# Optimization experiments

Measured on AMD Instinct MI355X. Metric: run time of the kernel, lower is better.

## Reference

```python
import jax, jax.numpy as jnp
import numpy as np

LMAX = 3
D_IRREP = (LMAX + 1) ** 2  # 16
EPS = 1e-5


def _conv1d(x, w, pad):
    # x: [N, C_in, L], w: [C_out, C_in, K] -> [N, C_out, L]
    return jax.lax.conv_general_dilated(
        x, w, window_strides=(1,), padding=[(pad, pad)],
        dimension_numbers=("NCH", "OIH", "NCH"))


def setup_inputs() -> dict:
    key = jax.random.key(0)
    ks = jax.random.split(key, 8)
    B, Cin, Cout, N, K, RES = 128, 256, 256, 64, 5, 8
    return {
        "x": jax.random.normal(ks[0], (B, Cin * D_IRREP, N), jnp.float32),
        "weight": jax.random.normal(ks[1], (LMAX + 1, Cout, Cin, K), jnp.float32) / np.sqrt(Cin * K).astype(np.float32),
        "bias": jax.random.normal(ks[2], (1, 1, Cout), jnp.float32) * 0.02,
        "affine_weight": jnp.ones((LMAX + 1, Cout), jnp.float32),
        "gating_w": jax.random.normal(ks[3], (Cout, Cout), jnp.float32) / np.sqrt(Cout).astype(np.float32),
        "gating_b": jnp.zeros((Cout,), jnp.float32),
        "to_grid": jax.random.normal(ks[4], (RES, RES, D_IRREP), jnp.float32) * 0.3,
        "from_grid": jax.random.normal(ks[5], (RES, RES, D_IRREP), jnp.float32) * 0.3,
    }


def reference(x, weight, bias, affine_weight, gating_w, gating_b, to_grid, from_grid):
    B, CI, N = x.shape
    Cin = CI // D_IRREP
    Cout = weight.shape[1]
    pad = weight.shape[-1] // 2
    x = x.reshape(B, Cin, D_IRREP, N)

    # per-degree Conv1d over the time axis, irrep order folded into batch
    h_parts = []
    for l in range(LMAX + 1):
        lo, li = l * l, 2 * l + 1
        x_l = x[:, :, lo:lo + li, :]                                  # [B, Cin, li, N]
        x_l = x_l.transpose(0, 2, 1, 3).reshape(B * li, Cin, N)       # (b i) c n
        h_l = _conv1d(x_l, weight[l], pad)                            # [B*li, Cout, N]
        h_l = h_l.reshape(B, li, Cout, N).transpose(0, 3, 1, 2).reshape(B * N, li, Cout)  # (b n) i c
        if l == 0:
            h_l = h_l + bias
        h_parts.append(h_l)
    h = jnp.concatenate(h_parts, axis=1)                              # [B*N, 16, Cout]

    # rms_norm_sh: center l=0 over channels, degree-balanced RMS, per-degree affine
    degrees = np.repeat(np.arange(LMAX + 1), 2 * np.arange(LMAX + 1) + 1)  # [16]
    bal = jnp.asarray((1.0 / (2.0 * degrees + 1.0)) / (LMAX + 1), h.dtype)  # [16]
    mean0 = jnp.mean(h[:, :1, :], axis=2, keepdims=True)
    h = jnp.concatenate([h[:, :1, :] - mean0, h[:, 1:, :]], axis=1)
    var = jnp.einsum("zic,i->zc", h * h, bal)                         # [Z, C]
    inv = jax.lax.rsqrt(jnp.mean(var, axis=-1)[:, None, None] + EPS)  # [Z,1,1]
    h = h * inv * affine_weight[degrees][None]                        # [Z,16,C]

    # SeparableS2Activation: SiLU-gated scalars + S2 grid activation for l>0
    gate = jax.nn.silu(h[:, :1, :] @ gating_w.T + gating_b)           # [Z,1,C]
    grid = jax.nn.silu(jnp.einsum("bai,zic->zbac", to_grid, h))       # [Z,8,8,C]
    s2 = jnp.einsum("bai,zbac->zic", from_grid, grid)                 # [Z,16,C]
    h = jnp.concatenate([gate, s2[:, 1:, :]], axis=1)

    # (b n) i c -> b (c i) n
    out = h.reshape(B, N, D_IRREP, Cout).transpose(0, 3, 2, 1).reshape(B, Cout * D_IRREP, N)
    return out
```

## Files before the change

### kernel.cpp

```cpp
#include <hip/hip_runtime.h>
#include <hip/hip_bf16.h>

#define BB    128
#define CIN   256
#define COUT  256
#define NN    64
#define KW    5
#define DIRR  16
#define ZTOT  (BB*NN)
#define SX    264

typedef __attribute__((ext_vector_type(4)))  float f32x4;
typedef __attribute__((ext_vector_type(16))) float f32x16;
typedef __attribute__((ext_vector_type(8)))  short s16x8;

__device__ inline ushort f2bf(float f) {
    __hip_bfloat16 h = __float2bfloat16(f);
    return *(const ushort*)&h;
}
__device__ inline float bf2f(ushort u) {
    union { unsigned int ui; float f; } cv; cv.ui = ((unsigned int)u) << 16;
    return cv.f;
}
__device__ inline float wave_sum(float v) {
    #pragma unroll
    for (int o = 32; o > 0; o >>= 1) v += __shfl_down(v, o, 64);
    return v;
}
__device__ inline float silu(float x) { return x / (1.f + __expf(-x)); }

__global__ __launch_bounds__(256) void pack_all_k(const float* __restrict__ w,
                                                  const float* __restrict__ gw,
                                                  const float* __restrict__ tg,
                                                  const float* __restrict__ fg,
                                                  ushort* __restrict__ wb,
                                                  ushort* __restrict__ gwb,
                                                  ushort* __restrict__ tgb,
                                                  ushort* __restrict__ fgTb)
{
    int idx = blockIdx.x * 256 + threadIdx.x;
    if (idx < 1310720) {
        int cl16 = idx & 15;
        int c    = (idx >> 4) & 255;
        int ch   = (idx >> 12) & 15;
        int lk   = idx >> 16;
        int k    = lk % 5;
        int l    = lk / 5;
        int cin  = ch * 16 + cl16;
        wb[idx] = f2bf(w[(((size_t)(l * COUT + c) * CIN) + cin) * KW + k]);
        return;
    }
    int j2 = idx - 1310720;
    if (j2 < 65536) {
        gwb[j2] = f2bf(gw[j2]);
    } else if (j2 < 66560) {
        int j = j2 - 65536;
        tgb[j] = f2bf(tg[j]);
    } else if (j2 < 67584) {
        int j = j2 - 66560;
        int p = j >> 4, i = j & 15;
        fgTb[i * 64 + p] = f2bf(fg[j]);
    }
}

__global__ __launch_bounds__(256, 4) void conv_mfma_k(const float* __restrict__ x,
                                                      const ushort* __restrict__ wb,
                                                      const float* __restrict__ bias,
                                                      ushort* __restrict__ hbuf)
{
    __shared__ __align__(16) ushort xs[68 * SX];

    const int tid  = threadIdx.x;
    const int lane = tid & 63;
    const int wid  = tid >> 6;
    const int blk  = blockIdx.x;
    const int b = blk >> 4, i = blk & 15;
    const int l = (i == 0) ? 0 : (i < 4) ? 1 : (i < 9) ? 2 : 3;

    {
        const float4* xb = (const float4*)(x + (((size_t)b * CIN) * DIRR + i) * NN);
        #pragma unroll
        for (int p = 0; p < 16; ++p) {
            int cin = (tid & 63) | ((p & 3) << 6);
            int nq  = ((tid >> 6) << 2) | (p >> 2);
            float4 v = xb[(size_t)cin * (DIRR * NN / 4) + nq];
            ushort* dst = xs + (size_t)(2 + nq * 4) * SX + cin;
            dst[0]      = f2bf(v.x);
            dst[SX]     = f2bf(v.y);
            dst[2 * SX] = f2bf(v.z);
            dst[3 * SX] = f2bf(v.w);
        }
        xs[ 0 * SX + tid] = 0; xs[ 1 * SX + tid] = 0;
        xs[66 * SX + tid] = 0; xs[67 * SX + tid] = 0;
    }
    __syncthreads();

    f32x16 acc[2][2];
    #pragma unroll
    for (int m = 0; m < 2; ++m)
        #pragma unroll
        for (int j = 0; j < 2; ++j)
            #pragma unroll
            for (int r = 0; r < 16; ++r) acc[m][j][r] = 0.f;

    const int l31 = lane & 31;
    const int kh  = lane >> 5;

    const ushort* wl = wb + (size_t)l * (80 * 4096);
    int boffB[2];
    #pragma unroll
    for (int j = 0; j < 2; ++j)
        boffB[j] = (wid * 64 + j * 32 + l31) * 16 + kh * 8;

    const ushort* arow = xs + (size_t)l31 * SX + kh * 8;

#define LOADB(dst, t) do {                                              \
        const ushort* bt_ = wl + ((size_t)(t) << 12);                   \
        dst##0 = *(const s16x8*)(bt_ + boffB[0]);                       \
        dst##1 = *(const s16x8*)(bt_ + boffB[1]);                       \
    } while (0)

#define MSTEP(bv, t) do {                                               \
        const ushort* ab_ = arow + (size_t)((t) >> 4) * SX + ((t) & 15) * 16; \
        s16x8 av0_ = *(const s16x8*)(ab_);                              \
        s16x8 av1_ = *(const s16x8*)(ab_ + (size_t)32 * SX);            \
        acc[0][0] = __builtin_amdgcn_mfma_f32_32x32x16_bf16(av0_, bv##0, acc[0][0], 0, 0, 0); \
        acc[0][1] = __builtin_amdgcn_mfma_f32_32x32x16_bf16(av0_, bv##1, acc[0][1], 0, 0, 0); \
        acc[1][0] = __builtin_amdgcn_mfma_f32_32x32x16_bf16(av1_, bv##0, acc[1][0], 0, 0, 0); \
        acc[1][1] = __builtin_amdgcn_mfma_f32_32x32x16_bf16(av1_, bv##1, acc[1][1], 0, 0, 0); \
    } while (0)

    s16x8 s0_0, s0_1, s1_0, s1_1, s2_0, s2_1, s3_0, s3_1;
    LOADB(s0_, 0);
    LOADB(s1_, 1);
    LOADB(s2_, 2);
    LOADB(s3_, 3);

    #pragma unroll 1
    for (int t = 0; t < 80; t += 4) {
        MSTEP(s0_, t);
        if (t + 4 < 80) LOADB(s0_, t + 4);
        MSTEP(s1_, t + 1);
        if (t + 5 < 80) LOADB(s1_, t + 5);
        MSTEP(s2_, t + 2);
        if (t + 6 < 80) LOADB(s2_, t + 6);
        MSTEP(s3_, t + 3);
        if (t + 7 < 80) LOADB(s3_, t + 7);
    }
#undef LOADB
#undef MSTEP

    #pragma unroll
    for (int j = 0; j < 2; ++j) {
        int c = wid * 64 + j * 32 + l31;
        float bvv = (i == 0) ? bias[c] : 0.f;
        #pragma unroll
        for (int m = 0; m < 2; ++m)
            #pragma unroll
            for (int r = 0; r < 16; ++r) {
                int n = m * 32 + (r & 3) + 8 * (r >> 2) + 4 * kh;
                size_t z = (size_t)b * NN + n;
                hbuf[(z * DIRR + i) * COUT + c] = f2bf(acc[m][j][r] + bvv);
            }
    }
}

__global__ __launch_bounds__(256) void norm_k(const ushort* __restrict__ hbuf,
                                              const float* __restrict__ afw,
                                              ushort* __restrict__ hn2,
                                              ushort* __restrict__ hn0)
{
    __shared__ float red[16];
    const int z0 = blockIdx.x * 4;
    const int c = threadIdx.x;
    const int lane = c & 63, w = c >> 6;

    float hv[4][16];
    #pragma unroll
    for (int zz = 0; zz < 4; ++zz)
        #pragma unroll
        for (int i = 0; i < 16; ++i)
            hv[zz][i] = bf2f(hbuf[((size_t)(z0 + zz) * DIRR + i) * COUT + c]);

    float s[4];
    #pragma unroll
    for (int zz = 0; zz < 4; ++zz) s[zz] = wave_sum(hv[zz][0]);
    if (lane == 0) {
        #pragma unroll
        for (int zz = 0; zz < 4; ++zz) red[zz * 4 + w] = s[zz];
    }
    __syncthreads();
    #pragma unroll
    for (int zz = 0; zz < 4; ++zz) {
        float m = (red[zz * 4] + red[zz * 4 + 1] + red[zz * 4 + 2] + red[zz * 4 + 3]) * (1.f / 256.f);
        hv[zz][0] -= m;
    }

    const float bal[4] = {0.25f, 1.f / 12.f, 1.f / 20.f, 1.f / 28.f};
    float var[4];
    #pragma unroll
    for (int zz = 0; zz < 4; ++zz) {
        float v = bal[0] * hv[zz][0] * hv[zz][0];
        #pragma unroll
        for (int i = 1; i < 16; ++i) {
            int li = (i < 4) ? 1 : (i < 9) ? 2 : 3;
            v += bal[li] * hv[zz][i] * hv[zz][i];
        }
        var[zz] = wave_sum(v);
    }
    __syncthreads();
    if (lane == 0) {
        #pragma unroll
        for (int zz = 0; zz < 4; ++zz) red[zz * 4 + w] = var[zz];
    }
    __syncthreads();
    float inv[4];
    #pragma unroll
    for (int zz = 0; zz < 4; ++zz)
        inv[zz] = rsqrtf((red[zz * 4] + red[zz * 4 + 1] + red[zz * 4 + 2] + red[zz * 4 + 3]) * (1.f / 256.f) + 1e-5f);

    float a0 = afw[c], a1 = afw[COUT + c], a2 = afw[2 * COUT + c], a3 = afw[3 * COUT + c];
    #pragma unroll
    for (int zz = 0; zz < 4; ++zz) {
        s16x8 o0, o1;
        #pragma unroll
        for (int i = 0; i < 16; ++i) {
            float al = (i == 0) ? a0 : (i < 4) ? a1 : (i < 9) ? a2 : a3;
            ushort ub = f2bf(hv[zz][i] * inv[zz] * al);
            if (i < 8) o0[i] = (short)ub; else o1[i - 8] = (short)ub;
        }
        ushort* dst = hn2 + ((size_t)c * ZTOT + z0 + zz) * DIRR;
        *(s16x8*)dst = o0;
        *(s16x8*)(dst + 8) = o1;
        hn0[(size_t)(z0 + zz) * COUT + c] = (ushort)(unsigned short)o0[0];
    }
}

__global__ __launch_bounds__(256) void gate_k(const ushort* __restrict__ hn0,
                                              const ushort* __restrict__ gwb,
                                              const float* __restrict__ gb,
                                              float* __restrict__ out)
{
    const int b = blockIdx.x;
    const int tid = threadIdx.x;
    const int lane = tid & 63, w = tid >> 6;
    const int lr = lane & 15, kb = lane >> 4;

    f32x4 acc[4][4];
    #pragma unroll
    for (int m = 0; m < 4; ++m)
        #pragma unroll
        for (int n = 0; n < 4; ++n) acc[m][n] = (f32x4){0.f, 0.f, 0.f, 0.f};

    #pragma unroll 1
    for (int ks = 0; ks < 8; ++ks) {
        s16x8 av[4], bv[4];
        #pragma unroll
        for (int m = 0; m < 4; ++m)
            av[m] = *(const s16x8*)(hn0 + ((size_t)(b * 64 + m * 16 + lr) * 256 + ks * 32 + kb * 8));
        #pragma unroll
        for (int n = 0; n < 4; ++n)
            bv[n] = *(const s16x8*)(gwb + ((size_t)(w * 64 + n * 16 + lr) * 256 + ks * 32 + kb * 8));
        #pragma unroll
        for (int m = 0; m < 4; ++m)
            #pragma unroll
            for (int n = 0; n < 4; ++n)
                acc[m][n] = __builtin_amdgcn_mfma_f32_16x16x32_bf16(av[m], bv[n], acc[m][n], 0, 0, 0);
    }

    #pragma unroll
    for (int n = 0; n < 4; ++n) {
        int c = w * 64 + n * 16 + lr;
        float gbc = gb[c];
        #pragma unroll
        for (int m = 0; m < 4; ++m)
            #pragma unroll
            for (int r = 0; r < 4; ++r) {
                int nrow = m * 16 + kb * 4 + r;
                out[((size_t)b * COUT + c) * (DIRR * NN) + nrow] = silu(acc[m][n][r] + gbc);
            }
    }
}

__global__ __launch_bounds__(256) void grid_k(const ushort* __restrict__ hn2,
                                              const ushort* __restrict__ tgb,
                                              const ushort* __restrict__ fgTb,
                                              float* __restrict__ out)
{
    __shared__ __align__(16) char lds[36864 + 2048 + 2304];
    ushort* P_s  = (ushort*)lds;
    float*  S_s  = (float*)lds;
    ushort* tg_s = (ushort*)(lds + 36864);
    ushort* fgT_s= (ushort*)(lds + 36864 + 2048);

    const int bid = blockIdx.x;
    const int c  = bid & 255;
    const int zt = bid >> 8;
    const int z0 = zt * 256;
    const int tid = threadIdx.x;
    const int lane = tid & 63, w = tid >> 6;
    const int lr = lane & 15, kb = lane >> 4;

    #pragma unroll
    for (int q = 0; q < 4; ++q) {
        int idx = q * 256 + tid;
        tg_s[idx] = tgb[idx];
        int i = idx >> 6, p = idx & 63;
        fgT_s[i * 72 + p] = fgTb[idx];
    }
    __syncthreads();

    f32x4 acc[4][4];
    #pragma unroll
    for (int m = 0; m < 4; ++m)
        #pragma unroll
        for (int n = 0; n < 4; ++n) acc[m][n] = (f32x4){0.f, 0.f, 0.f, 0.f};

    s16x8 bv[4];
    #pragma unroll
    for (int n = 0; n < 4; ++n)
        bv[n] = (kb < 2) ? *(const s16x8*)(tg_s + (n * 16 + lr) * 16 + kb * 8)
                         : (s16x8){0,0,0,0,0,0,0,0};
    #pragma unroll
    for (int m = 0; m < 4; ++m) {
        int zl = w * 64 + m * 16 + lr;
        s16x8 av = (kb < 2) ? *(const s16x8*)(hn2 + ((size_t)c * ZTOT + z0 + zl) * DIRR + kb * 8)
                            : (s16x8){0,0,0,0,0,0,0,0};
        #pragma unroll
        for (int n = 0; n < 4; ++n)
            acc[m][n] = __builtin_amdgcn_mfma_f32_16x16x32_bf16(av, bv[n], acc[m][n], 0, 0, 0);
    }

    #pragma unroll
    for (int m = 0; m < 4; ++m)
        #pragma unroll
        for (int n = 0; n < 4; ++n)
            #pragma unroll
            for (int r = 0; r < 4; ++r) {
                int zl = w * 64 + m * 16 + kb * 4 + r;
                int p  = n * 16 + lr;
                P_s[zl * 72 + p] = f2bf(silu(acc[m][n][r]));
            }

    f32x4 acc2[4];
    #pragma unroll
    for (int m = 0; m < 4; ++m) acc2[m] = (f32x4){0.f, 0.f, 0.f, 0.f};
    #pragma unroll
    for (int ks = 0; ks < 2; ++ks) {
        s16x8 bv2 = *(const s16x8*)(fgT_s + lr * 72 + ks * 32 + kb * 8);
        #pragma unroll
        for (int m = 0; m < 4; ++m) {
            s16x8 av2 = *(const s16x8*)(P_s + (w * 64 + m * 16 + lr) * 72 + ks * 32 + kb * 8);
            acc2[m] = __builtin_amdgcn_mfma_f32_16x16x32_bf16(av2, bv2, acc2[m], 0, 0, 0);
        }
    }

    __syncthreads();

    #pragma unroll
    for (int m = 0; m < 4; ++m)
        #pragma unroll
        for (int r = 0; r < 4; ++r) {
            int zl = w * 64 + m * 16 + kb * 4 + r;
            S_s[zl * 17 + lr] = acc2[m][r];
        }
    __syncthreads();

    const int bb = tid >> 6, n = tid & 63;
    const int b0 = zt * 4;
    const float* srow = S_s + (bb * 64 + n) * 17;
    float* obase = out + ((size_t)(b0 + bb) * COUT + c) * (DIRR * NN) + n;
    #pragma unroll
    for (int i = 1; i < 16; ++i)
        obase[i * NN] = srow[i];
}

__global__ __launch_bounds__(256) void post_k(const ushort* __restrict__ hbuf,
                                              const float* __restrict__ afw,
                                              const float* __restrict__ gw,
                                              const float* __restrict__ gb,
                                              const float* __restrict__ tg,
                                              const float* __restrict__ fg,
                                              float* __restrict__ out)
{
    __shared__ float h0s[COUT];
    __shared__ float red[4];
    __shared__ float tgs[64 * 16];
    __shared__ float fgs[64 * 16];

    int z = blockIdx.x;
    int c = threadIdx.x;
    int b = z >> 6, n = z & 63;
    int lane = c & 63, wid = c >> 6;

    for (int idx = c; idx < 1024; idx += 256) { tgs[idx] = tg[idx]; fgs[idx] = fg[idx]; }

    float hv[16];
    #pragma unroll
    for (int i = 0; i < 16; ++i)
        hv[i] = bf2f(hbuf[((size_t)z * DIRR + i) * COUT + c]);

    float s0 = wave_sum(hv[0]);
    if (lane == 0) red[wid] = s0;
    __syncthreads();
    float mean0 = (red[0] + red[1] + red[2] + red[3]) * (1.f / 256.f);
    hv[0] -= mean0;

    const float bal[4] = {0.25f, 1.f / 12.f, 1.f / 20.f, 1.f / 28.f};
    float var = bal[0] * hv[0] * hv[0];
    #pragma unroll
    for (int i = 1; i < 16; ++i) {
        int li = (i < 4) ? 1 : (i < 9) ? 2 : 3;
        var += bal[li] * hv[i] * hv[i];
    }
    float s1 = wave_sum(var);
    __syncthreads();
    if (lane == 0) red[wid] = s1;
    __syncthreads();
    float inv = rsqrtf((red[0] + red[1] + red[2] + red[3]) * (1.f / 256.f) + 1e-5f);

    float a0 = afw[c], a1 = afw[COUT + c], a2 = afw[2 * COUT + c], a3 = afw[3 * COUT + c];
    #pragma unroll
    for (int i = 0; i < 16; ++i) {
        float al = (i == 0) ? a0 : (i < 4) ? a1 : (i < 9) ? a2 : a3;
        hv[i] *= inv * al;
    }
    h0s[c] = hv[0];
    __syncthreads();

    float g = gb[c];
    const float4* gwr = (const float4*)(gw + (size_t)c * COUT);
    #pragma unroll 4
    for (int j = 0; j < 64; ++j) {
        float4 wv = gwr[j];
        g += h0s[4 * j] * wv.x + h0s[4 * j + 1] * wv.y + h0s[4 * j + 2] * wv.z + h0s[4 * j + 3] * wv.w;
    }
    float gate = silu(g);

    float s2a[16];
    #pragma unroll
    for (int i = 0; i < 16; ++i) s2a[i] = 0.f;
    #pragma unroll 1
    for (int p = 0; p < 64; ++p) {
        float gv = 0.f;
        #pragma unroll
        for (int i = 0; i < 16; ++i) gv += tgs[p * 16 + i] * hv[i];
        gv = silu(gv);
        #pragma unroll
        for (int i = 0; i < 16; ++i) s2a[i] += fgs[p * 16 + i] * gv;
    }

    float* ob = out + (size_t)b * COUT * DIRR * NN + (size_t)c * DIRR * NN + n;
    ob[0] = gate;
    #pragma unroll
    for (int i = 1; i < 16; ++i) ob[i * NN] = s2a[i];
}

extern "C" void kernel_launch(void* const* d_in, const int* in_sizes, int n_in,
                              void* d_out, int out_size, void* d_ws, size_t ws_size,
                              hipStream_t stream)
{
    const float* x    = (const float*)d_in[0];
    const float* w    = (const float*)d_in[1];
    const float* bias = (const float*)d_in[2];
    const float* afw  = (const float*)d_in[3];
    const float* gw   = (const float*)d_in[4];
    const float* gb   = (const float*)d_in[5];
    const float* tg   = (const float*)d_in[6];
    const float* fg   = (const float*)d_in[7];
    float* out = (float*)d_out;

    const size_t off_hbuf = 0;
    const size_t off_wb   = 67108864;
    const size_t off_hn2  = 69730304;
    const size_t off_hn0  = off_hn2 + 67108864;
    const size_t off_gwb  = off_hn0 + 4194304;
    const size_t off_tgb  = off_gwb + 131072;
    const size_t off_fgT  = off_tgb + 2048;
    const size_t need     = off_fgT + 2048;

    ushort* hbuf = (ushort*)((char*)d_ws + off_hbuf);
    ushort* wb   = (ushort*)((char*)d_ws + off_wb);

    if (ws_size >= need) {
        ushort* hn2  = (ushort*)((char*)d_ws + off_hn2);
        ushort* hn0  = (ushort*)((char*)d_ws + off_hn0);
        ushort* gwb  = (ushort*)((char*)d_ws + off_gwb);
        ushort* tgb  = (ushort*)((char*)d_ws + off_tgb);
        ushort* fgTb = (ushort*)((char*)d_ws + off_fgT);

        pack_all_k <<<5384, 256, 0, stream>>>(w, gw, tg, fg, wb, gwb, tgb, fgTb);
        conv_mfma_k<<<BB * DIRR, 256, 0, stream>>>(x, wb, bias, hbuf);
        norm_k     <<<ZTOT / 4, 256, 0, stream>>>(hbuf, afw, hn2, hn0);
        gate_k     <<<BB, 256, 0, stream>>>(hn0, gwb, gb, out);
        grid_k     <<<256 * (ZTOT / 256), 256, 0, stream>>>(hn2, tgb, fgTb, out);
    } else {
        pack_all_k <<<5120, 256, 0, stream>>>(w, gw, tg, fg, wb,
                                              (ushort*)((char*)d_ws + off_wb),
                                              (ushort*)((char*)d_ws + off_wb),
                                              (ushort*)((char*)d_ws + off_wb));
        conv_mfma_k<<<BB * DIRR, 256, 0, stream>>>(x, wb, bias, hbuf);
        post_k     <<<ZTOT, 256, 0, stream>>>(hbuf, afw, gw, gb, tg, fg, out);
    }
}
```

Baseline: 248.8 us.

## Process two batches per conv block to share weight fragments across MFMAs

The conv MFMA kernel now stages two batch elements' input slices in LDS, with 512 threads per block and half as many blocks. Each wave covers 32 output channels. Each weight fragment loaded from global memory is reused across both batches instead of across two channel tiles. This halves global weight loads per MFMA, at the cost of twice as many LDS A-fragment reads and double the shared-memory footprint per block, which may limit how many blocks fit on a CU.

```diff
diff --git a/kernel.cpp b/kernel.cpp
--- a/kernel.cpp
+++ b/kernel.cpp
@@ -63,74 +63,80 @@
     }
 }
 
-__global__ __launch_bounds__(256, 4) void conv_mfma_k(const float* __restrict__ x,
+__global__ __launch_bounds__(512, 4) void conv_mfma_k(const float* __restrict__ x,
                                                       const ushort* __restrict__ wb,
                                                       const float* __restrict__ bias,
                                                       ushort* __restrict__ hbuf)
 {
-    __shared__ __align__(16) ushort xs[68 * SX];
+    __shared__ __align__(16) ushort xs[2 * 68 * SX];
 
     const int tid  = threadIdx.x;
     const int lane = tid & 63;
     const int wid  = tid >> 6;
     const int blk  = blockIdx.x;
-    const int b = blk >> 4, i = blk & 15;
+    const int bp = blk >> 4, i = blk & 15;
+    const int b0 = bp * 2;
     const int l = (i == 0) ? 0 : (i < 4) ? 1 : (i < 9) ? 2 : 3;
 
     {
-        const float4* xb = (const float4*)(x + (((size_t)b * CIN) * DIRR + i) * NN);
+        const int bb = tid >> 8;
+        const int t8 = tid & 255;
+        const float4* xb = (const float4*)(x + (((size_t)(b0 + bb) * CIN) * DIRR + i) * NN);
+        ushort* xp = xs + (size_t)bb * 68 * SX;
         #pragma unroll
         for (int p = 0; p < 16; ++p) {
-            int cin = (tid & 63) | ((p & 3) << 6);
-            int nq  = ((tid >> 6) << 2) | (p >> 2);
+            int cin = (t8 & 63) | ((p & 3) << 6);
+            int nq  = ((t8 >> 6) << 2) | (p >> 2);
             float4 v = xb[(size_t)cin * (DIRR * NN / 4) + nq];
-            ushort* dst = xs + (size_t)(2 + nq * 4) * SX + cin;
+            ushort* dst = xp + (size_t)(2 + nq * 4) * SX + cin;
             dst[0]      = f2bf(v.x);
             dst[SX]     = f2bf(v.y);
             dst[2 * SX] = f2bf(v.z);
             dst[3 * SX] = f2bf(v.w);
         }
-        xs[ 0 * SX + tid] = 0; xs[ 1 * SX + tid] = 0;
-        xs[66 * SX + tid] = 0; xs[67 * SX + tid] = 0;
+        for (int idx2 = tid; idx2 < 2 * 4 * SX; idx2 += 512) {
+            int pb  = idx2 >= 4 * SX;
+            int rem = idx2 - pb * 4 * SX;
+            int r4  = rem / SX;
+            int col = rem - r4 * SX;
+            int row = (r4 < 2) ? r4 : (64 + r4);
+            xs[((size_t)pb * 68 + row) * SX + col] = 0;
+        }
     }
     __syncthreads();
 
     f32x16 acc[2][2];
     #pragma unroll
-    for (int m = 0; m < 2; ++m)
-        #pragma unroll
-        for (int j = 0; j < 2; ++j)
+    for (int bq = 0; bq < 2; ++bq)
+        #pragma unroll
+        for (int m = 0; m < 2; ++m)
             #pragma unroll
-            for (int r = 0; r < 16; ++r) acc[m][j][r] = 0.f;
+            for (int r = 0; r < 16; ++r) acc[bq][m][r] = 0.f;
 
     const int l31 = lane & 31;
     const int kh  = lane >> 5;
 
     const ushort* wl = wb + (size_t)l * (80 * 4096);
-    int boffB[2];
-    #pragma unroll
-    for (int j = 0; j < 2; ++j)
-        boffB[j] = (wid * 64 + j * 32 + l31) * 16 + kh * 8;
-
+    const int boffB = (wid * 32 + l31) * 16 + kh * 8;
     const ushort* arow = xs + (size_t)l31 * SX + kh * 8;
 
 #define LOADB(dst, t) do {                                              \
-        const ushort* bt_ = wl + ((size_t)(t) << 12);                   \
-        dst##0 = *(const s16x8*)(bt_ + boffB[0]);                       \
-        dst##1 = *(const s16x8*)(bt_ + boffB[1]);                       \
+        dst = *(const s16x8*)(wl + ((size_t)(t) << 12) + boffB);        \
     } while (0)
 
 #define MSTEP(bv, t) do {                                               \
         const ushort* ab_ = arow + (size_t)((t) >> 4) * SX + ((t) & 15) * 16; \
-        s16x8 av0_ = *(const s16x8*)(ab_);                              \
-        s16x8 av1_ = *(const s16x8*)(ab_ + (size_t)32 * SX);            \
-        acc[0][0] = __builtin_amdgcn_mfma_f32_32x32x16_bf16(av0_, bv##0, acc[0][0], 0, 0, 0); \
-        acc[0][1] = __builtin_amdgcn_mfma_f32_32x32x16_bf16(av0_, bv##1, acc[0][1], 0, 0, 0); \
-        acc[1][0] = __builtin_amdgcn_mfma_f32_32x32x16_bf16(av1_, bv##0, acc[1][0], 0, 0, 0); \
-        acc[1][1] = __builtin_amdgcn_mfma_f32_32x32x16_bf16(av1_, bv##1, acc[1][1], 0, 0, 0); \
+        s16x8 a00_ = *(const s16x8*)(ab_);                              \
+        s16x8 a01_ = *(const s16x8*)(ab_ + (size_t)32 * SX);            \
+        s16x8 a10_ = *(const s16x8*)(ab_ + (size_t)68 * SX);            \
+        s16x8 a11_ = *(const s16x8*)(ab_ + (size_t)100 * SX);           \
+        acc[0][0] = __builtin_amdgcn_mfma_f32_32x32x16_bf16(a00_, bv, acc[0][0], 0, 0, 0); \
+        acc[0][1] = __builtin_amdgcn_mfma_f32_32x32x16_bf16(a01_, bv, acc[0][1], 0, 0, 0); \
+        acc[1][0] = __builtin_amdgcn_mfma_f32_32x32x16_bf16(a10_, bv, acc[1][0], 0, 0, 0); \
+        acc[1][1] = __builtin_amdgcn_mfma_f32_32x32x16_bf16(a11_, bv, acc[1][1], 0, 0, 0); \
     } while (0)
 
-    s16x8 s0_0, s0_1, s1_0, s1_1, s2_0, s2_1, s3_0, s3_1;
+    s16x8 s0_, s1_, s2_, s3_;
     LOADB(s0_, 0);
     LOADB(s1_, 1);
     LOADB(s2_, 2);
@@ -150,19 +156,18 @@
 #undef LOADB
 #undef MSTEP
 
-    #pragma unroll
-    for (int j = 0; j < 2; ++j) {
-        int c = wid * 64 + j * 32 + l31;
-        float bvv = (i == 0) ? bias[c] : 0.f;
+    const int c = wid * 32 + l31;
+    const float bvv = (i == 0) ? bias[c] : 0.f;
+    #pragma unroll
+    for (int bq = 0; bq < 2; ++bq)
         #pragma unroll
         for (int m = 0; m < 2; ++m)
             #pragma unroll
             for (int r = 0; r < 16; ++r) {
                 int n = m * 32 + (r & 3) + 8 * (r >> 2) + 4 * kh;
-                size_t z = (size_t)b * NN + n;
-                hbuf[(z * DIRR + i) * COUT + c] = f2bf(acc[m][j][r] + bvv);
+                size_t z = (size_t)(b0 + bq) * NN + n;
+                hbuf[(z * DIRR + i) * COUT + c] = f2bf(acc[bq][m][r] + bvv);
             }
-    }
 }
 
 __global__ __launch_bounds__(256) void norm_k(const ushort* __restrict__ hbuf,
@@ -490,7 +495,7 @@
         ushort* fgTb = (ushort*)((char*)d_ws + off_fgT);
 
         pack_all_k <<<5384, 256, 0, stream>>>(w, gw, tg, fg, wb, gwb, tgb, fgTb);
-        conv_mfma_k<<<BB * DIRR, 256, 0, stream>>>(x, wb, bias, hbuf);
+        conv_mfma_k<<<(BB / 2) * DIRR, 512, 0, stream>>>(x, wb, bias, hbuf);
         norm_k     <<<ZTOT / 4, 256, 0, stream>>>(hbuf, afw, hn2, hn0);
         gate_k     <<<BB, 256, 0, stream>>>(hn0, gwb, gb, out);
         grid_k     <<<256 * (ZTOT / 256), 256, 0, stream>>>(hn2, tgb, fgTb, out);
@@ -499,7 +504,7 @@
                                               (ushort*)((char*)d_ws + off_wb),
                                               (ushort*)((char*)d_ws + off_wb),
                                               (ushort*)((char*)d_ws + off_wb));
-        conv_mfma_k<<<BB * DIRR, 256, 0, stream>>>(x, wb, bias, hbuf);
+        conv_mfma_k<<<(BB / 2) * DIRR, 512, 0, stream>>>(x, wb, bias, hbuf);
         post_k     <<<ZTOT, 256, 0, stream>>>(hbuf, afw, gw, gb, tg, fg, out);
     }
 }
```

New measurement: 240.3 us (median of 2 runs). -3.4%, faster.
